# Kernel tuning notes

Measured on AMD Instinct MI355X. Metric: run time of the kernel, lower is better.

The kernel has to match this reference:

```python
import jax, jax.numpy as jnp
import numpy as np

B, N, C, H = 8192, 36, 128, 8
HD = C // H  # 16
FOCUS = 3
EPS = 1e-4


def setup_inputs() -> dict:
    key = jax.random.key(0)
    ks = jax.random.split(key, 10)
    x = jax.random.normal(ks[0], (B, N, C), dtype=jnp.float32)
    pos = jax.random.normal(ks[1], (B, N, C), dtype=jnp.float32)
    mask = jax.random.randint(ks[2], (B, N), 0, 2).astype(jnp.float32)
    coords = jax.random.randint(ks[3], (B * N, 4), 0, 8).astype(jnp.int64)
    voxel_inds = jax.random.permutation(ks[4], B * N).reshape(B, N).astype(jnp.int64)
    s = 0.02
    qk_w = jax.random.normal(ks[5], (C, 2 * C), dtype=jnp.float32) * s
    qk_b = jnp.zeros((2 * C,), dtype=jnp.float32)
    v_w = jax.random.normal(ks[6], (C, C), dtype=jnp.float32) * s
    v_b = jnp.zeros((C,), dtype=jnp.float32)
    proj_w = jax.random.normal(ks[7], (C, C), dtype=jnp.float32) * s
    proj_b = jnp.zeros((C,), dtype=jnp.float32)
    return {"x": x, "pos": pos, "mask": mask, "qk_w": qk_w, "qk_b": qk_b,
            "v_w": v_w, "v_b": v_b, "proj_w": proj_w, "proj_b": proj_b,
            "coords": coords, "voxel_inds": voxel_inds}


def reference(x, pos, mask, qk_w, qk_b, v_w, v_b, proj_w, proj_b, coords, voxel_inds):
    b, n, c = x.shape
    qk = (x + pos) @ qk_w + qk_b                      # (B,N,2C)
    q, k = qk[..., :c], qk[..., c:]
    v = x @ v_w + v_b                                 # (B,N,C)
    k = k * mask[..., None]
    # split heads -> (B,H,N,HD)
    q = q.reshape(b, n, H, HD).transpose(0, 2, 1, 3)
    k = k.reshape(b, n, H, HD).transpose(0, 2, 1, 3)
    v = v.reshape(b, n, H, HD).transpose(0, 2, 1, 3)
    # focusing power
    q = q ** FOCUS
    k = k ** FOCUS
    # q normalized per-token over channels; k normalized per-channel over tokens
    # (original rearranges k to (bh, c, n) before norm(dim=-1))
    q = q / (EPS + jnp.linalg.norm(q, axis=-1, keepdims=True))
    k = k / (EPS + jnp.linalg.norm(k, axis=2, keepdims=True))
    # linear attention: kv = k^T v (HD x HD), then q @ kv
    kv = jnp.einsum('bhnc,bhnd->bhcd', k, v)          # (B,H,HD,HD)
    out = jnp.einsum('bhnc,bhcd->bhnd', q, kv)        # (B,H,N,HD)
    out = out.transpose(0, 2, 1, 3).reshape(b, n, c)  # (B,N,C)
    num = jnp.sum(mask, axis=-1, keepdims=True)       # (B,1)
    out = out / (num[..., None] + EPS)
    # inverse-permutation gather: perm[voxel_inds.flat] = arange
    flat = voxel_inds.reshape(-1)
    M = coords.shape[0]
    perm = jnp.zeros((M,), dtype=flat.dtype).at[flat].set(
        jnp.arange(M, dtype=flat.dtype))
    out = out.reshape(-1, c)[perm]                    # (M,C)
    out = out @ proj_w + proj_b
    return out
```

## Files before the change

### kernel.cpp

```cpp
#include <hip/hip_runtime.h>

typedef __bf16 bf16x8 __attribute__((ext_vector_type(8)));
typedef float f32x4 __attribute__((ext_vector_type(4)));

#define Bdim 8192
#define Nn 36
#define Cc 128
#define EPSf 1e-4f

#define WS_QK_HI 0
#define WS_QK_LO 32768
#define WS_V_HI  65536
#define WS_P_HI  81920

#define OFF_XH   0
#define OFF_PH   12288
#define OFF_PL   24576
#define OFF_KT   0
#define OFF_VT   12288
#define OFF_QH   24576
#define OFF_KV   33792
#define OFF_O    0
#define OFF_MASK 39936
#define OFF_VOX  40128
#define OFF_INN  40272
#define LDS_BYTES 40448

__device__ inline uint bfh(float f) {
    __bf16 h = (__bf16)f;
    return (uint)(*(const ushort*)&h);
}
__device__ inline uint bfl(float f) {
    float hf = (float)((__bf16)f);
    __bf16 l = (__bf16)(f - hf);
    return (uint)(*(const ushort*)&l);
}
__device__ inline uint pk2h(float a, float b) { return bfh(a) | (bfh(b) << 16); }
__device__ inline uint pk2l(float a, float b) { return bfl(a) | (bfl(b) << 16); }

union U8 { bf16x8 v; uint u[4]; };

__global__ __launch_bounds__(256)
void prep_frags(const float* __restrict__ qk_w, const float* __restrict__ v_w,
                const float* __restrict__ proj_w, ushort* __restrict__ ws)
{
    int e = blockIdx.x * 256 + threadIdx.x;
    const float* W; int N; int idx; int hi_off; int lo_off;
    if (e < 32768)      { W = qk_w;   N = 256; hi_off = WS_QK_HI; lo_off = WS_QK_LO; idx = e; }
    else if (e < 49152) { W = v_w;    N = 128; hi_off = WS_V_HI;  lo_off = -1;       idx = e - 32768; }
    else                { W = proj_w; N = 128; hi_off = WS_P_HI;  lo_off = -1;       idx = e - 49152; }
    int j    = idx & 7;
    int lane = (idx >> 3) & 63;
    int ks   = (idx >> 9) & 3;
    int ct   = idx >> 11;
    int col  = ct * 16 + (lane & 15);
    int k    = ks * 32 + (lane >> 4) * 8 + j;
    float v  = W[k * N + col];
    ws[hi_off + idx] = (ushort)bfh(v);
    if (lo_off >= 0) ws[lo_off + idx] = (ushort)bfl(v);
}

__global__ __launch_bounds__(512, 6)
void fla_mfma(const float* __restrict__ x, const float* __restrict__ pos,
              const float* __restrict__ mask, const float* __restrict__ qk_b,
              const float* __restrict__ v_b, const float* __restrict__ proj_b,
              const int* __restrict__ vox, const ushort* __restrict__ ws,
              float* __restrict__ out)
{
    __shared__ __align__(16) char lds[LDS_BYTES];
    const int t = threadIdx.x;
    const int b = blockIdx.x;
    const int lane = t & 63;
    const int wv = t >> 6;

    const int  rsel = lane & 15;
    const int  grp  = lane >> 4;
    const uint kgrp = (uint)grp * 8u;
    const uint sw   = ((uint)rsel) << 4;

    const float* xg = x + (size_t)b * (Nn * Cc);
    const float* pg = pos + (size_t)b * (Nn * Cc);
    #pragma unroll
    for (int it = 0; it < 3; ++it) {
        int idx = t + it * 512;
        int n = idx >> 5;
        int c4 = (idx & 31) << 2;
        float4 xv = make_float4(0.f, 0.f, 0.f, 0.f);
        float4 pv = make_float4(0.f, 0.f, 0.f, 0.f);
        if (n < Nn) {
            xv = *(const float4*)(xg + n * Cc + c4);
            pv = *(const float4*)(pg + n * Cc + c4);
        }
        float s0 = xv.x + pv.x, s1 = xv.y + pv.y, s2 = xv.z + pv.z, s3 = xv.w + pv.w;
        uint ba = (uint)n * 256u + (((uint)(c4 * 2)) ^ (((uint)n & 15u) << 4));
        *(uint2*)(lds + OFF_XH + ba) = make_uint2(pk2h(xv.x, xv.y), pk2h(xv.z, xv.w));
        *(uint2*)(lds + OFF_PH + ba) = make_uint2(pk2h(s0, s1), pk2h(s2, s3));
        *(uint2*)(lds + OFF_PL + ba) = make_uint2(pk2l(s0, s1), pk2l(s2, s3));
    }
    if (t < 48) ((float*)(lds + OFF_MASK))[t] = (t < Nn) ? mask[(size_t)b * Nn + t] : 0.f;
    if (t >= 64 && t < 64 + Nn) ((int*)(lds + OFF_VOX))[t - 64] = vox[(size_t)b * Nn + (t - 64)];
    if (t == 128) {
        float s = 0.f;
        for (int n = 0; n < Nn; ++n) s += mask[(size_t)b * Nn + n];
        *(float*)(lds + OFF_INN) = 1.f / (s + EPSf);
    }
    __syncthreads();

    f32x4 accV[3];
    f32x4 accQ[3][2];
    #pragma unroll
    for (int rt = 0; rt < 3; ++rt) {
        accV[rt] = (f32x4){0.f, 0.f, 0.f, 0.f};
        accQ[rt][0] = (f32x4){0.f, 0.f, 0.f, 0.f};
        accQ[rt][1] = (f32x4){0.f, 0.f, 0.f, 0.f};
    }
    #pragma unroll
    for (int ks = 0; ks < 4; ++ks) {
        uint ka = (((uint)(ks * 32) + kgrp) * 2u) ^ sw;
        bf16x8 xh[3];
        #pragma unroll
        for (int rt = 0; rt < 3; ++rt)
            xh[rt] = *(const bf16x8*)(lds + OFF_XH + (uint)(rt * 16 + rsel) * 256u + ka);
        int f = ((wv * 4 + ks) * 64 + lane) * 8;
        bf16x8 bvh = *(const bf16x8*)(ws + WS_V_HI + f);
        #pragma unroll
        for (int rt = 0; rt < 3; ++rt)
            accV[rt] = __builtin_amdgcn_mfma_f32_16x16x32_bf16(xh[rt], bvh, accV[rt], 0, 0, 0);
    }
    #pragma unroll
    for (int ks = 0; ks < 4; ++ks) {
        uint ka = (((uint)(ks * 32) + kgrp) * 2u) ^ sw;
        bf16x8 ph[3], pl[3];
        #pragma unroll
        for (int rt = 0; rt < 3; ++rt) {
            uint ba = (uint)(rt * 16 + rsel) * 256u + ka;
            ph[rt] = *(const bf16x8*)(lds + OFF_PH + ba);
            pl[rt] = *(const bf16x8*)(lds + OFF_PL + ba);
        }
        #pragma unroll
        for (int ci = 0; ci < 2; ++ci) {
            int f = (((wv * 2 + ci) * 4 + ks) * 64 + lane) * 8;
            bf16x8 bh = *(const bf16x8*)(ws + WS_QK_HI + f);
            bf16x8 bl = *(const bf16x8*)(ws + WS_QK_LO + f);
            #pragma unroll
            for (int rt = 0; rt < 3; ++rt) {
                accQ[rt][ci] = __builtin_amdgcn_mfma_f32_16x16x32_bf16(ph[rt], bh, accQ[rt][ci], 0, 0, 0);
                accQ[rt][ci] = __builtin_amdgcn_mfma_f32_16x16x32_bf16(ph[rt], bl, accQ[rt][ci], 0, 0, 0);
                accQ[rt][ci] = __builtin_amdgcn_mfma_f32_16x16x32_bf16(pl[rt], bh, accQ[rt][ci], 0, 0, 0);
            }
        }
    }
    __syncthreads();

    const float* sM = (const float*)(lds + OFF_MASK);
    {
        int colv = wv * 16 + rsel;
        float vb = v_b[colv];
        #pragma unroll
        for (int rt = 0; rt < 3; ++rt) {
            float a0 = accV[rt][0] + vb, a1 = accV[rt][1] + vb;
            float a2 = accV[rt][2] + vb, a3 = accV[rt][3] + vb;
            uint addr = OFF_VT + (uint)(colv * 48 + rt * 16 + grp * 4) * 2u;
            *(uint2*)(lds + addr) = make_uint2(pk2h(a0, a1), pk2h(a2, a3));
        }
    }
    if (wv < 4) {
        #pragma unroll
        for (int ci = 0; ci < 2; ++ci) {
            int colq = (wv * 2 + ci) * 16 + rsel;
            float qb = qk_b[colq];
            uint cb2 = (uint)(colq * 2);
            #pragma unroll
            for (int rt = 0; rt < 3; ++rt) {
                #pragma unroll
                for (int r = 0; r < 4; ++r) {
                    int row = rt * 16 + grp * 4 + r;
                    if (row < Nn) {
                        float q1 = accQ[rt][ci][r] + qb;
                        float q3 = q1 * q1 * q1;
                        uint ba = (uint)row * 256u + (cb2 ^ (((uint)row & 15u) << 4));
                        *(ushort*)(lds + OFF_QH + ba) = (ushort)bfh(q3);
                    }
                }
            }
        }
    } else {
        #pragma unroll
        for (int ci = 0; ci < 2; ++ci) {
            int colk = ((wv - 4) * 2 + ci) * 16 + rsel;
            float kb = qk_b[Cc + colk];
            #pragma unroll
            for (int rt = 0; rt < 3; ++rt) {
                float k3v[4];
                #pragma unroll
                for (int r = 0; r < 4; ++r) {
                    int row = rt * 16 + grp * 4 + r;
                    float k1 = (accQ[rt][ci][r] + kb) * sM[row];
                    k3v[r] = k1 * k1 * k1;
                }
                uint addr = OFF_KT + (uint)(colk * 48 + rt * 16 + grp * 4) * 2u;
                *(uint2*)(lds + addr) = make_uint2(pk2h(k3v[0], k3v[1]), pk2h(k3v[2], k3v[3]));
            }
        }
    }
    __syncthreads();

    {
        int col16 = wv * 16 + rsel;
        uint a0 = OFF_KT + (uint)(col16 * 48 + grp * 8) * 2u;
        uint b0 = OFF_VT + (uint)(col16 * 48 + grp * 8) * 2u;
        bf16x8 kA0 = *(const bf16x8*)(lds + a0);
        bf16x8 vB0 = *(const bf16x8*)(lds + b0);
        U8 kA1, vB1;
        kA1.u[0] = kA1.u[1] = kA1.u[2] = kA1.u[3] = 0u;
        vB1.u[0] = vB1.u[1] = vB1.u[2] = vB1.u[3] = 0u;
        if (grp < 2) {
            kA1.v = *(const bf16x8*)(lds + a0 + 64);
            vB1.v = *(const bf16x8*)(lds + b0 + 64);
        }
        float s = 0.f;
        #pragma unroll
        for (int j = 0; j < 8; ++j) { float q = (float)kA0[j]; s += q * q; }
        #pragma unroll
        for (int j = 0; j < 8; ++j) { float q = (float)kA1.v[j]; s += q * q; }
        s += __shfl_xor(s, 16);
        s += __shfl_xor(s, 32);
        float invkn = 1.f / (EPSf + sqrtf(s));

        f32x4 kvacc = (f32x4){0.f, 0.f, 0.f, 0.f};
        kvacc = __builtin_amdgcn_mfma_f32_16x16x32_bf16(kA0, vB0, kvacc, 0, 0, 0);
        kvacc = __builtin_amdgcn_mfma_f32_16x16x32_bf16(kA1.v, vB1.v, kvacc, 0, 0, 0);

        float f0 = __shfl(invkn, grp * 4 + 0);
        float f1 = __shfl(invkn, grp * 4 + 1);
        float f2 = __shfl(invkn, grp * 4 + 2);
        float f3 = __shfl(invkn, grp * 4 + 3);
        uint addr = OFF_KV + (uint)(wv * 384 + rsel * 24 + grp * 4) * 2u;
        *(uint2*)(lds + addr) =
            make_uint2(pk2h(kvacc[0] * f0, kvacc[1] * f1), pk2h(kvacc[2] * f2, kvacc[3] * f3));
    }
    __syncthreads();

    {
        int d = rsel;
        float inn = *(const float*)(lds + OFF_INN);
        U8 bkv;
        bkv.u[0] = bkv.u[1] = bkv.u[2] = bkv.u[3] = 0u;
        if (grp < 2)
            bkv.v = *(const bf16x8*)(lds + OFF_KV + (uint)(wv * 384 + d * 24 + grp * 8) * 2u);
        f32x4 oacc[3];
        float invn[3];
        #pragma unroll
        for (int rt = 0; rt < 3; ++rt) {
            int row = rt * 16 + rsel;
            U8 aq;
            aq.u[0] = aq.u[1] = aq.u[2] = aq.u[3] = 0u;
            if (grp < 2 && row < Nn) {
                uint ba = (uint)row * 256u +
                          (((uint)((wv * 16 + grp * 8) * 2)) ^ (((uint)row & 15u) << 4));
                aq.v = *(const bf16x8*)(lds + OFF_QH + ba);
            }
            float s = 0.f;
            #pragma unroll
            for (int j = 0; j < 8; ++j) { float q = (float)aq.v[j]; s += q * q; }
            s += __shfl_xor(s, 16);
            invn[rt] = 1.f / (EPSf + sqrtf(s));
            f32x4 o = (f32x4){0.f, 0.f, 0.f, 0.f};
            o = __builtin_amdgcn_mfma_f32_16x16x32_bf16(aq.v, bkv.v, o, 0, 0, 0);
            oacc[rt] = o;
        }
        #pragma unroll
        for (int rt = 0; rt < 3; ++rt) {
            #pragma unroll
            for (int r = 0; r < 4; ++r) {
                int rr = grp * 4 + r;
                int row = rt * 16 + rr;
                float fac = __shfl(invn[rt], rr) * inn;
                float val = oacc[rt][r] * fac;
                uint ba = (uint)row * 256u +
                          (((uint)((wv * 16 + d) * 2)) ^ (((uint)row & 15u) << 4));
                *(ushort*)(lds + OFF_O + ba) = (ushort)bfh(val);
            }
        }
    }
    __syncthreads();

    f32x4 accP[3];
    #pragma unroll
    for (int rt = 0; rt < 3; ++rt) accP[rt] = (f32x4){0.f, 0.f, 0.f, 0.f};
    #pragma unroll
    for (int ks = 0; ks < 4; ++ks) {
        uint ka = (((uint)(ks * 32) + kgrp) * 2u) ^ sw;
        bf16x8 oa[3];
        #pragma unroll
        for (int rt = 0; rt < 3; ++rt)
            oa[rt] = *(const bf16x8*)(lds + OFF_O + (uint)(rt * 16 + rsel) * 256u + ka);
        int f = ((wv * 4 + ks) * 64 + lane) * 8;
        bf16x8 bp = *(const bf16x8*)(ws + WS_P_HI + f);
        #pragma unroll
        for (int rt = 0; rt < 3; ++rt)
            accP[rt] = __builtin_amdgcn_mfma_f32_16x16x32_bf16(oa[rt], bp, accP[rt], 0, 0, 0);
    }
    {
        const int* sVx = (const int*)(lds + OFF_VOX);
        int col = wv * 16 + rsel;
        float pb = proj_b[col];
        #pragma unroll
        for (int rt = 0; rt < 3; ++rt) {
            #pragma unroll
            for (int r = 0; r < 4; ++r) {
                int row = rt * 16 + grp * 4 + r;
                if (row < Nn)
                    out[(size_t)sVx[row] * Cc + col] = accP[rt][r] + pb;
            }
        }
    }
}

extern "C" void kernel_launch(void* const* d_in, const int* in_sizes, int n_in,
                              void* d_out, int out_size, void* d_ws, size_t ws_size,
                              hipStream_t stream) {
    (void)in_sizes; (void)n_in; (void)out_size; (void)ws_size;
    const float* x      = (const float*)d_in[0];
    const float* pos    = (const float*)d_in[1];
    const float* mask   = (const float*)d_in[2];
    const float* qk_w   = (const float*)d_in[3];
    const float* qk_b   = (const float*)d_in[4];
    const float* v_w    = (const float*)d_in[5];
    const float* v_b    = (const float*)d_in[6];
    const float* proj_w = (const float*)d_in[7];
    const float* proj_b = (const float*)d_in[8];
    const int*   vox    = (const int*)d_in[10];
    ushort* ws = (ushort*)d_ws;
    float* outp = (float*)d_out;

    hipLaunchKernelGGL(prep_frags, dim3(256), dim3(256), 0, stream, qk_w, v_w, proj_w, ws);
    hipLaunchKernelGGL(fla_mfma, dim3(Bdim), dim3(512), 0, stream,
                       x, pos, mask, qk_b, v_b, proj_b, vox, ws, outp);
}
```

Before: 218.9 us.

## Process two batches per block with staggered double-buffered LDS phases

Each block now handles two batch items, each with its own LDS buffer, and interleaves their phases so one item's global loads and MFMA work overlap the other's epilogue stages. This halves the grid and shares barriers across both items, reducing per-item sync cost. The KV scratch stride shrinks to fit two buffers, padding rows are zeroed once up front, and launch bounds drop to 4 waves per SIMD, trading occupancy and register pressure for in-block overlap.

```diff
diff --git a/kernel.cpp b/kernel.cpp
--- a/kernel.cpp
+++ b/kernel.cpp
@@ -21,10 +21,10 @@
 #define OFF_QH   24576
 #define OFF_KV   33792
 #define OFF_O    0
-#define OFF_MASK 39936
-#define OFF_VOX  40128
-#define OFF_INN  40272
-#define LDS_BYTES 40448
+#define OFF_MASK 38912
+#define OFF_VOX  39104
+#define OFF_INN  39248
+#define AST      39296
 
 __device__ inline uint bfh(float f) {
     __bf16 h = (__bf16)f;
@@ -60,16 +60,15 @@
     if (lo_off >= 0) ws[lo_off + idx] = (ushort)bfl(v);
 }
 
-__global__ __launch_bounds__(512, 6)
+__global__ __launch_bounds__(512, 4)
 void fla_mfma(const float* __restrict__ x, const float* __restrict__ pos,
               const float* __restrict__ mask, const float* __restrict__ qk_b,
               const float* __restrict__ v_b, const float* __restrict__ proj_b,
               const int* __restrict__ vox, const ushort* __restrict__ ws,
               float* __restrict__ out)
 {
-    __shared__ __align__(16) char lds[LDS_BYTES];
+    __shared__ __align__(16) char lds[2][AST];
     const int t = threadIdx.x;
-    const int b = blockIdx.x;
     const int lane = t & 63;
     const int wv = t >> 6;
 
@@ -78,145 +77,152 @@
     const uint kgrp = (uint)grp * 8u;
     const uint sw   = ((uint)rsel) << 4;
 
-    const float* xg = x + (size_t)b * (Nn * Cc);
-    const float* pg = pos + (size_t)b * (Nn * Cc);
-    #pragma unroll
-    for (int it = 0; it < 3; ++it) {
-        int idx = t + it * 512;
-        int n = idx >> 5;
-        int c4 = (idx & 31) << 2;
-        float4 xv = make_float4(0.f, 0.f, 0.f, 0.f);
-        float4 pv = make_float4(0.f, 0.f, 0.f, 0.f);
-        if (n < Nn) {
-            xv = *(const float4*)(xg + n * Cc + c4);
-            pv = *(const float4*)(pg + n * Cc + c4);
-        }
-        float s0 = xv.x + pv.x, s1 = xv.y + pv.y, s2 = xv.z + pv.z, s3 = xv.w + pv.w;
-        uint ba = (uint)n * 256u + (((uint)(c4 * 2)) ^ (((uint)n & 15u) << 4));
-        *(uint2*)(lds + OFF_XH + ba) = make_uint2(pk2h(xv.x, xv.y), pk2h(xv.z, xv.w));
-        *(uint2*)(lds + OFF_PH + ba) = make_uint2(pk2h(s0, s1), pk2h(s2, s3));
-        *(uint2*)(lds + OFF_PL + ba) = make_uint2(pk2l(s0, s1), pk2l(s2, s3));
-    }
-    if (t < 48) ((float*)(lds + OFF_MASK))[t] = (t < Nn) ? mask[(size_t)b * Nn + t] : 0.f;
-    if (t >= 64 && t < 64 + Nn) ((int*)(lds + OFF_VOX))[t - 64] = vox[(size_t)b * Nn + (t - 64)];
-    if (t == 128) {
-        float s = 0.f;
-        for (int n = 0; n < Nn; ++n) s += mask[(size_t)b * Nn + n];
-        *(float*)(lds + OFF_INN) = 1.f / (s + EPSf);
-    }
-    __syncthreads();
-
-    f32x4 accV[3];
-    f32x4 accQ[3][2];
-    #pragma unroll
-    for (int rt = 0; rt < 3; ++rt) {
-        accV[rt] = (f32x4){0.f, 0.f, 0.f, 0.f};
-        accQ[rt][0] = (f32x4){0.f, 0.f, 0.f, 0.f};
-        accQ[rt][1] = (f32x4){0.f, 0.f, 0.f, 0.f};
-    }
-    #pragma unroll
-    for (int ks = 0; ks < 4; ++ks) {
-        uint ka = (((uint)(ks * 32) + kgrp) * 2u) ^ sw;
-        bf16x8 xh[3];
-        #pragma unroll
-        for (int rt = 0; rt < 3; ++rt)
-            xh[rt] = *(const bf16x8*)(lds + OFF_XH + (uint)(rt * 16 + rsel) * 256u + ka);
-        int f = ((wv * 4 + ks) * 64 + lane) * 8;
-        bf16x8 bvh = *(const bf16x8*)(ws + WS_V_HI + f);
-        #pragma unroll
-        for (int rt = 0; rt < 3; ++rt)
-            accV[rt] = __builtin_amdgcn_mfma_f32_16x16x32_bf16(xh[rt], bvh, accV[rt], 0, 0, 0);
-    }
-    #pragma unroll
-    for (int ks = 0; ks < 4; ++ks) {
-        uint ka = (((uint)(ks * 32) + kgrp) * 2u) ^ sw;
-        bf16x8 ph[3], pl[3];
+    const int b0 = blockIdx.x * 2;
+    const int b1 = b0 + 1;
+
+    auto PA = [&](int ar, int bb) {
+        char* L = lds[ar];
+        const float* xg = x + (size_t)bb * (Nn * Cc);
+        const float* pg = pos + (size_t)bb * (Nn * Cc);
+        #pragma unroll
+        for (int it = 0; it < 3; ++it) {
+            int idx = t + it * 512;
+            if (idx < Nn * 32) {
+                int n = idx >> 5;
+                int c4 = (idx & 31) << 2;
+                float4 xv = *(const float4*)(xg + n * Cc + c4);
+                float4 pv = *(const float4*)(pg + n * Cc + c4);
+                float s0 = xv.x + pv.x, s1 = xv.y + pv.y;
+                float s2 = xv.z + pv.z, s3 = xv.w + pv.w;
+                uint ba = (uint)n * 256u + (((uint)(c4 * 2)) ^ (((uint)n & 15u) << 4));
+                *(uint2*)(L + OFF_XH + ba) = make_uint2(pk2h(xv.x, xv.y), pk2h(xv.z, xv.w));
+                *(uint2*)(L + OFF_PH + ba) = make_uint2(pk2h(s0, s1), pk2h(s2, s3));
+                *(uint2*)(L + OFF_PL + ba) = make_uint2(pk2l(s0, s1), pk2l(s2, s3));
+            }
+        }
+        if (t < 48) ((float*)(L + OFF_MASK))[t] = (t < Nn) ? mask[(size_t)bb * Nn + t] : 0.f;
+        if (t >= 64 && t < 64 + Nn) ((int*)(L + OFF_VOX))[t - 64] = vox[(size_t)bb * Nn + (t - 64)];
+        if (t == 128) {
+            float s = 0.f;
+            for (int n = 0; n < Nn; ++n) s += mask[(size_t)bb * Nn + n];
+            *(float*)(L + OFF_INN) = 1.f / (s + EPSf);
+        }
+    };
+
+    auto PB = [&](int ar, f32x4 (&accV)[3], f32x4 (&accQ)[3][2]) {
+        char* L = lds[ar];
         #pragma unroll
         for (int rt = 0; rt < 3; ++rt) {
-            uint ba = (uint)(rt * 16 + rsel) * 256u + ka;
-            ph[rt] = *(const bf16x8*)(lds + OFF_PH + ba);
-            pl[rt] = *(const bf16x8*)(lds + OFF_PL + ba);
-        }
-        #pragma unroll
-        for (int ci = 0; ci < 2; ++ci) {
-            int f = (((wv * 2 + ci) * 4 + ks) * 64 + lane) * 8;
-            bf16x8 bh = *(const bf16x8*)(ws + WS_QK_HI + f);
-            bf16x8 bl = *(const bf16x8*)(ws + WS_QK_LO + f);
+            accV[rt] = (f32x4){0.f, 0.f, 0.f, 0.f};
+            accQ[rt][0] = (f32x4){0.f, 0.f, 0.f, 0.f};
+            accQ[rt][1] = (f32x4){0.f, 0.f, 0.f, 0.f};
+        }
+        #pragma unroll
+        for (int ks = 0; ks < 4; ++ks) {
+            uint ka = (((uint)(ks * 32) + kgrp) * 2u) ^ sw;
+            bf16x8 xh[3];
+            #pragma unroll
+            for (int rt = 0; rt < 3; ++rt)
+                xh[rt] = *(const bf16x8*)(L + OFF_XH + (uint)(rt * 16 + rsel) * 256u + ka);
+            int f = ((wv * 4 + ks) * 64 + lane) * 8;
+            bf16x8 bvh = *(const bf16x8*)(ws + WS_V_HI + f);
+            #pragma unroll
+            for (int rt = 0; rt < 3; ++rt)
+                accV[rt] = __builtin_amdgcn_mfma_f32_16x16x32_bf16(xh[rt], bvh, accV[rt], 0, 0, 0);
+        }
+        #pragma unroll
+        for (int ks = 0; ks < 4; ++ks) {
+            uint ka = (((uint)(ks * 32) + kgrp) * 2u) ^ sw;
+            bf16x8 ph[3], pl[3];
             #pragma unroll
             for (int rt = 0; rt < 3; ++rt) {
-                accQ[rt][ci] = __builtin_amdgcn_mfma_f32_16x16x32_bf16(ph[rt], bh, accQ[rt][ci], 0, 0, 0);
-                accQ[rt][ci] = __builtin_amdgcn_mfma_f32_16x16x32_bf16(ph[rt], bl, accQ[rt][ci], 0, 0, 0);
-                accQ[rt][ci] = __builtin_amdgcn_mfma_f32_16x16x32_bf16(pl[rt], bh, accQ[rt][ci], 0, 0, 0);
-            }
-        }
-    }
-    __syncthreads();
-
-    const float* sM = (const float*)(lds + OFF_MASK);
-    {
-        int colv = wv * 16 + rsel;
-        float vb = v_b[colv];
-        #pragma unroll
-        for (int rt = 0; rt < 3; ++rt) {
-            float a0 = accV[rt][0] + vb, a1 = accV[rt][1] + vb;
-            float a2 = accV[rt][2] + vb, a3 = accV[rt][3] + vb;
-            uint addr = OFF_VT + (uint)(colv * 48 + rt * 16 + grp * 4) * 2u;
-            *(uint2*)(lds + addr) = make_uint2(pk2h(a0, a1), pk2h(a2, a3));
-        }
-    }
-    if (wv < 4) {
-        #pragma unroll
-        for (int ci = 0; ci < 2; ++ci) {
-            int colq = (wv * 2 + ci) * 16 + rsel;
-            float qb = qk_b[colq];
-            uint cb2 = (uint)(colq * 2);
+                uint ba = (uint)(rt * 16 + rsel) * 256u + ka;
+                ph[rt] = *(const bf16x8*)(L + OFF_PH + ba);
+                pl[rt] = *(const bf16x8*)(L + OFF_PL + ba);
+            }
+            #pragma unroll
+            for (int ci = 0; ci < 2; ++ci) {
+                int f = (((wv * 2 + ci) * 4 + ks) * 64 + lane) * 8;
+                bf16x8 bh = *(const bf16x8*)(ws + WS_QK_HI + f);
+                bf16x8 bl = *(const bf16x8*)(ws + WS_QK_LO + f);
+                #pragma unroll
+                for (int rt = 0; rt < 3; ++rt) {
+                    accQ[rt][ci] = __builtin_amdgcn_mfma_f32_16x16x32_bf16(ph[rt], bh, accQ[rt][ci], 0, 0, 0);
+                    accQ[rt][ci] = __builtin_amdgcn_mfma_f32_16x16x32_bf16(ph[rt], bl, accQ[rt][ci], 0, 0, 0);
+                    accQ[rt][ci] = __builtin_amdgcn_mfma_f32_16x16x32_bf16(pl[rt], bh, accQ[rt][ci], 0, 0, 0);
+                }
+            }
+        }
+    };
+
+    auto PC = [&](int ar, f32x4 (&accV)[3], f32x4 (&accQ)[3][2]) {
+        char* L = lds[ar];
+        const float* sM = (const float*)(L + OFF_MASK);
+        {
+            int colv = wv * 16 + rsel;
+            float vb = v_b[colv];
             #pragma unroll
             for (int rt = 0; rt < 3; ++rt) {
+                float a0 = accV[rt][0] + vb, a1 = accV[rt][1] + vb;
+                float a2 = accV[rt][2] + vb, a3 = accV[rt][3] + vb;
+                uint addr = OFF_VT + (uint)(colv * 48 + rt * 16 + grp * 4) * 2u;
+                *(uint2*)(L + addr) = make_uint2(pk2h(a0, a1), pk2h(a2, a3));
+            }
+        }
+        if (wv < 4) {
+            #pragma unroll
+            for (int ci = 0; ci < 2; ++ci) {
+                int colq = (wv * 2 + ci) * 16 + rsel;
+                float qb = qk_b[colq];
+                uint cb2 = (uint)(colq * 2);
                 #pragma unroll
-                for (int r = 0; r < 4; ++r) {
-                    int row = rt * 16 + grp * 4 + r;
-                    if (row < Nn) {
-                        float q1 = accQ[rt][ci][r] + qb;
-                        float q3 = q1 * q1 * q1;
-                        uint ba = (uint)row * 256u + (cb2 ^ (((uint)row & 15u) << 4));
-                        *(ushort*)(lds + OFF_QH + ba) = (ushort)bfh(q3);
+                for (int rt = 0; rt < 3; ++rt) {
+                    #pragma unroll
+                    for (int r = 0; r < 4; ++r) {
+                        int row = rt * 16 + grp * 4 + r;
+                        if (row < Nn) {
+                            float q1 = accQ[rt][ci][r] + qb;
+                            float q3 = q1 * q1 * q1;
+                            uint ba = (uint)row * 256u + (cb2 ^ (((uint)row & 15u) << 4));
+                            *(ushort*)(L + OFF_QH + ba) = (ushort)bfh(q3);
+                        }
                     }
                 }
             }
-        }
-    } else {
-        #pragma unroll
-        for (int ci = 0; ci < 2; ++ci) {
-            int colk = ((wv - 4) * 2 + ci) * 16 + rsel;
-            float kb = qk_b[Cc + colk];
-            #pragma unroll
-            for (int rt = 0; rt < 3; ++rt) {
-                float k3v[4];
+        } else {
+            #pragma unroll
+            for (int ci = 0; ci < 2; ++ci) {
+                int colk = ((wv - 4) * 2 + ci) * 16 + rsel;
+                float kb = qk_b[Cc + colk];
                 #pragma unroll
-                for (int r = 0; r < 4; ++r) {
-                    int row = rt * 16 + grp * 4 + r;
-                    float k1 = (accQ[rt][ci][r] + kb) * sM[row];
-                    k3v[r] = k1 * k1 * k1;
+                for (int rt = 0; rt < 3; ++rt) {
+                    float k3v[4];
+                    #pragma unroll
+                    for (int r = 0; r < 4; ++r) {
+                        int row = rt * 16 + grp * 4 + r;
+                        float k1 = (accQ[rt][ci][r] + kb) * sM[row];
+                        k3v[r] = k1 * k1 * k1;
+                    }
+                    uint addr = OFF_KT + (uint)(colk * 48 + rt * 16 + grp * 4) * 2u;
+                    *(uint2*)(L + addr) = make_uint2(pk2h(k3v[0], k3v[1]), pk2h(k3v[2], k3v[3]));
                 }
-                uint addr = OFF_KT + (uint)(colk * 48 + rt * 16 + grp * 4) * 2u;
-                *(uint2*)(lds + addr) = make_uint2(pk2h(k3v[0], k3v[1]), pk2h(k3v[2], k3v[3]));
-            }
-        }
-    }
-    __syncthreads();
-
-    {
+            }
+        }
+    };
+
+    auto PD = [&](int ar) {
+        char* L = lds[ar];
         int col16 = wv * 16 + rsel;
         uint a0 = OFF_KT + (uint)(col16 * 48 + grp * 8) * 2u;
-        uint b0 = OFF_VT + (uint)(col16 * 48 + grp * 8) * 2u;
-        bf16x8 kA0 = *(const bf16x8*)(lds + a0);
-        bf16x8 vB0 = *(const bf16x8*)(lds + b0);
+        uint b0_ = OFF_VT + (uint)(col16 * 48 + grp * 8) * 2u;
+        bf16x8 kA0 = *(const bf16x8*)(L + a0);
+        bf16x8 vB0 = *(const bf16x8*)(L + b0_);
         U8 kA1, vB1;
         kA1.u[0] = kA1.u[1] = kA1.u[2] = kA1.u[3] = 0u;
         vB1.u[0] = vB1.u[1] = vB1.u[2] = vB1.u[3] = 0u;
         if (grp < 2) {
-            kA1.v = *(const bf16x8*)(lds + a0 + 64);
-            vB1.v = *(const bf16x8*)(lds + b0 + 64);
+            kA1.v = *(const bf16x8*)(L + a0 + 64);
+            vB1.v = *(const bf16x8*)(L + b0_ + 64);
         }
         float s = 0.f;
         #pragma unroll
@@ -235,19 +241,19 @@
         float f1 = __shfl(invkn, grp * 4 + 1);
         float f2 = __shfl(invkn, grp * 4 + 2);
         float f3 = __shfl(invkn, grp * 4 + 3);
-        uint addr = OFF_KV + (uint)(wv * 384 + rsel * 24 + grp * 4) * 2u;
-        *(uint2*)(lds + addr) =
+        uint addr = OFF_KV + (uint)(wv * 320 + rsel * 20 + grp * 4) * 2u;
+        *(uint2*)(L + addr) =
             make_uint2(pk2h(kvacc[0] * f0, kvacc[1] * f1), pk2h(kvacc[2] * f2, kvacc[3] * f3));
-    }
-    __syncthreads();
-
-    {
+    };
+
+    auto PE = [&](int ar) {
+        char* L = lds[ar];
         int d = rsel;
-        float inn = *(const float*)(lds + OFF_INN);
+        float inn = *(const float*)(L + OFF_INN);
         U8 bkv;
         bkv.u[0] = bkv.u[1] = bkv.u[2] = bkv.u[3] = 0u;
         if (grp < 2)
-            bkv.v = *(const bf16x8*)(lds + OFF_KV + (uint)(wv * 384 + d * 24 + grp * 8) * 2u);
+            bkv.v = *(const bf16x8*)(L + OFF_KV + (uint)(wv * 320 + d * 20 + grp * 8) * 2u);
         f32x4 oacc[3];
         float invn[3];
         #pragma unroll
@@ -258,7 +264,7 @@
             if (grp < 2 && row < Nn) {
                 uint ba = (uint)row * 256u +
                           (((uint)((wv * 16 + grp * 8) * 2)) ^ (((uint)row & 15u) << 4));
-                aq.v = *(const bf16x8*)(lds + OFF_QH + ba);
+                aq.v = *(const bf16x8*)(L + OFF_QH + ba);
             }
             float s = 0.f;
             #pragma unroll
@@ -279,30 +285,30 @@
                 float val = oacc[rt][r] * fac;
                 uint ba = (uint)row * 256u +
                           (((uint)((wv * 16 + d) * 2)) ^ (((uint)row & 15u) << 4));
-                *(ushort*)(lds + OFF_O + ba) = (ushort)bfh(val);
-            }
-        }
-    }
-    __syncthreads();
-
-    f32x4 accP[3];
-    #pragma unroll
-    for (int rt = 0; rt < 3; ++rt) accP[rt] = (f32x4){0.f, 0.f, 0.f, 0.f};
-    #pragma unroll
-    for (int ks = 0; ks < 4; ++ks) {
-        uint ka = (((uint)(ks * 32) + kgrp) * 2u) ^ sw;
-        bf16x8 oa[3];
-        #pragma unroll
-        for (int rt = 0; rt < 3; ++rt)
-            oa[rt] = *(const bf16x8*)(lds + OFF_O + (uint)(rt * 16 + rsel) * 256u + ka);
-        int f = ((wv * 4 + ks) * 64 + lane) * 8;
-        bf16x8 bp = *(const bf16x8*)(ws + WS_P_HI + f);
-        #pragma unroll
-        for (int rt = 0; rt < 3; ++rt)
-            accP[rt] = __builtin_amdgcn_mfma_f32_16x16x32_bf16(oa[rt], bp, accP[rt], 0, 0, 0);
-    }
-    {
-        const int* sVx = (const int*)(lds + OFF_VOX);
+                *(ushort*)(L + OFF_O + ba) = (ushort)bfh(val);
+            }
+        }
+    };
+
+    auto PG = [&](int ar) {
+        char* L = lds[ar];
+        f32x4 accP[3];
+        #pragma unroll
+        for (int rt = 0; rt < 3; ++rt) accP[rt] = (f32x4){0.f, 0.f, 0.f, 0.f};
+        #pragma unroll
+        for (int ks = 0; ks < 4; ++ks) {
+            uint ka = (((uint)(ks * 32) + kgrp) * 2u) ^ sw;
+            bf16x8 oa[3];
+            #pragma unroll
+            for (int rt = 0; rt < 3; ++rt)
+                oa[rt] = *(const bf16x8*)(L + OFF_O + (uint)(rt * 16 + rsel) * 256u + ka);
+            int f = ((wv * 4 + ks) * 64 + lane) * 8;
+            bf16x8 bp = *(const bf16x8*)(ws + WS_P_HI + f);
+            #pragma unroll
+            for (int rt = 0; rt < 3; ++rt)
+                accP[rt] = __builtin_amdgcn_mfma_f32_16x16x32_bf16(oa[rt], bp, accP[rt], 0, 0, 0);
+        }
+        const int* sVx = (const int*)(L + OFF_VOX);
         int col = wv * 16 + rsel;
         float pb = proj_b[col];
         #pragma unroll
@@ -314,7 +320,37 @@
                     out[(size_t)sVx[row] * Cc + col] = accP[rt][r] + pb;
             }
         }
+    };
+
+    f32x4 accV0[3], accV1[3];
+    f32x4 accQ0[3][2], accQ1[3][2];
+
+    for (int i = t; i < 1152; i += 512) {
+        int ar = (i >= 576) ? 1 : 0;
+        int r3 = i - ar * 576;
+        char* rp = lds[ar] + (r3 < 192 ? OFF_XH : (r3 < 384 ? OFF_PH : OFF_PL));
+        int off = (r3 % 192) * 16 - (r3 < 192 ? 0 : (r3 < 384 ? 192 * 16 : 384 * 16)) + (r3 % 192) * 0;
+        off = ((r3 % 192) * 16);
+        *(uint4*)(rp + 9216 + off) = make_uint4(0u, 0u, 0u, 0u);
     }
+    PA(0, b0);
+    __syncthreads();
+    PB(0, accV0, accQ0);
+    PA(1, b1);
+    __syncthreads();
+    PC(0, accV0, accQ0);
+    PB(1, accV1, accQ1);
+    __syncthreads();
+    PD(0);
+    PC(1, accV1, accQ1);
+    __syncthreads();
+    PE(0);
+    PD(1);
+    __syncthreads();
+    PG(0);
+    PE(1);
+    __syncthreads();
+    PG(1);
 }
 
 extern "C" void kernel_launch(void* const* d_in, const int* in_sizes, int n_in,
@@ -335,6 +371,6 @@
     float* outp = (float*)d_out;
 
     hipLaunchKernelGGL(prep_frags, dim3(256), dim3(256), 0, stream, qk_w, v_w, proj_w, ws);
-    hipLaunchKernelGGL(fla_mfma, dim3(Bdim), dim3(512), 0, stream,
+    hipLaunchKernelGGL(fla_mfma, dim3(Bdim / 2), dim3(512), 0, stream,
                        x, pos, mask, qk_b, v_b, proj_b, vox, ws, outp);
 }
```

Measured after the change: 203.6 us. 7.0% less time.

## Halve block to 4 waves, double per-wave tiles, fuse kv and output stages

Applied to the files above, without the earlier changes.

Shrinks the fused attention block from 8 to 4 waves, so each wave computes twice as many column tiles in the QK, V and projection GEMMs and handles two heads in the attention step. The kv matrix is passed between lanes with shuffles instead of through shared memory, which removes one barrier and one LDS round trip. Padding rows are zeroed explicitly and the K/V transposed stride goes from 48 to 52 to reduce bank conflicts. The cost is more registers per thread and fewer waves per block to hide latency, though the launch bounds allow more blocks per CU.

```diff
diff --git a/kernel.cpp b/kernel.cpp
--- a/kernel.cpp
+++ b/kernel.cpp
@@ -17,10 +17,8 @@
 #define OFF_PH   12288
 #define OFF_PL   24576
 #define OFF_KT   0
-#define OFF_VT   12288
-#define OFF_QH   24576
-#define OFF_KV   33792
-#define OFF_O    0
+#define OFF_VT   13312
+#define OFF_QO   27648
 #define OFF_MASK 39936
 #define OFF_VOX  40128
 #define OFF_INN  40272
@@ -60,7 +58,7 @@
     if (lo_off >= 0) ws[lo_off + idx] = (ushort)bfl(v);
 }
 
-__global__ __launch_bounds__(512, 6)
+__global__ __launch_bounds__(256, 4)
 void fla_mfma(const float* __restrict__ x, const float* __restrict__ pos,
               const float* __restrict__ mask, const float* __restrict__ qk_b,
               const float* __restrict__ v_b, const float* __restrict__ proj_b,
@@ -72,7 +70,6 @@
     const int b = blockIdx.x;
     const int lane = t & 63;
     const int wv = t >> 6;
-
     const int  rsel = lane & 15;
     const int  grp  = lane >> 4;
     const uint kgrp = (uint)grp * 8u;
@@ -81,21 +78,31 @@
     const float* xg = x + (size_t)b * (Nn * Cc);
     const float* pg = pos + (size_t)b * (Nn * Cc);
     #pragma unroll
-    for (int it = 0; it < 3; ++it) {
-        int idx = t + it * 512;
-        int n = idx >> 5;
-        int c4 = (idx & 31) << 2;
-        float4 xv = make_float4(0.f, 0.f, 0.f, 0.f);
-        float4 pv = make_float4(0.f, 0.f, 0.f, 0.f);
-        if (n < Nn) {
-            xv = *(const float4*)(xg + n * Cc + c4);
-            pv = *(const float4*)(pg + n * Cc + c4);
-        }
-        float s0 = xv.x + pv.x, s1 = xv.y + pv.y, s2 = xv.z + pv.z, s3 = xv.w + pv.w;
-        uint ba = (uint)n * 256u + (((uint)(c4 * 2)) ^ (((uint)n & 15u) << 4));
-        *(uint2*)(lds + OFF_XH + ba) = make_uint2(pk2h(xv.x, xv.y), pk2h(xv.z, xv.w));
-        *(uint2*)(lds + OFF_PH + ba) = make_uint2(pk2h(s0, s1), pk2h(s2, s3));
-        *(uint2*)(lds + OFF_PL + ba) = make_uint2(pk2l(s0, s1), pk2l(s2, s3));
+    for (int i0 = 0; i0 < 3; ++i0) {
+        int i = t + i0 * 256;
+        if (i < 576) {
+            int reg = i / 192;
+            int j = i - reg * 192;
+            int row = 36 + (j >> 4);
+            int c16 = j & 15;
+            *(uint4*)(lds + reg * 12288 + row * 256 + c16 * 16) = make_uint4(0u, 0u, 0u, 0u);
+        }
+    }
+    #pragma unroll
+    for (int it = 0; it < 5; ++it) {
+        int idx = t + it * 256;
+        if (idx < Nn * 32) {
+            int n = idx >> 5;
+            int c4 = (idx & 31) << 2;
+            float4 xv = *(const float4*)(xg + n * Cc + c4);
+            float4 pv = *(const float4*)(pg + n * Cc + c4);
+            float s0 = xv.x + pv.x, s1 = xv.y + pv.y;
+            float s2 = xv.z + pv.z, s3 = xv.w + pv.w;
+            uint ba = (uint)n * 256u + (((uint)(c4 * 2)) ^ (((uint)n & 15u) << 4));
+            *(uint2*)(lds + OFF_XH + ba) = make_uint2(pk2h(xv.x, xv.y), pk2h(xv.z, xv.w));
+            *(uint2*)(lds + OFF_PH + ba) = make_uint2(pk2h(s0, s1), pk2h(s2, s3));
+            *(uint2*)(lds + OFF_PL + ba) = make_uint2(pk2l(s0, s1), pk2l(s2, s3));
+        }
     }
     if (t < 48) ((float*)(lds + OFF_MASK))[t] = (t < Nn) ? mask[(size_t)b * Nn + t] : 0.f;
     if (t >= 64 && t < 64 + Nn) ((int*)(lds + OFF_VOX))[t - 64] = vox[(size_t)b * Nn + (t - 64)];
@@ -106,26 +113,14 @@
     }
     __syncthreads();
 
-    f32x4 accV[3];
-    f32x4 accQ[3][2];
+    f32x4 accQ[3][4];
+    f32x4 accV[3][2];
     #pragma unroll
     for (int rt = 0; rt < 3; ++rt) {
-        accV[rt] = (f32x4){0.f, 0.f, 0.f, 0.f};
-        accQ[rt][0] = (f32x4){0.f, 0.f, 0.f, 0.f};
-        accQ[rt][1] = (f32x4){0.f, 0.f, 0.f, 0.f};
-    }
-    #pragma unroll
-    for (int ks = 0; ks < 4; ++ks) {
-        uint ka = (((uint)(ks * 32) + kgrp) * 2u) ^ sw;
-        bf16x8 xh[3];
-        #pragma unroll
-        for (int rt = 0; rt < 3; ++rt)
-            xh[rt] = *(const bf16x8*)(lds + OFF_XH + (uint)(rt * 16 + rsel) * 256u + ka);
-        int f = ((wv * 4 + ks) * 64 + lane) * 8;
-        bf16x8 bvh = *(const bf16x8*)(ws + WS_V_HI + f);
-        #pragma unroll
-        for (int rt = 0; rt < 3; ++rt)
-            accV[rt] = __builtin_amdgcn_mfma_f32_16x16x32_bf16(xh[rt], bvh, accV[rt], 0, 0, 0);
+        #pragma unroll
+        for (int ci = 0; ci < 4; ++ci) accQ[rt][ci] = (f32x4){0.f, 0.f, 0.f, 0.f};
+        accV[rt][0] = (f32x4){0.f, 0.f, 0.f, 0.f};
+        accV[rt][1] = (f32x4){0.f, 0.f, 0.f, 0.f};
     }
     #pragma unroll
     for (int ks = 0; ks < 4; ++ks) {
@@ -138,8 +133,8 @@
             pl[rt] = *(const bf16x8*)(lds + OFF_PL + ba);
         }
         #pragma unroll
-        for (int ci = 0; ci < 2; ++ci) {
-            int f = (((wv * 2 + ci) * 4 + ks) * 64 + lane) * 8;
+        for (int ci = 0; ci < 4; ++ci) {
+            int f = (((wv * 4 + ci) * 4 + ks) * 64 + lane) * 8;
             bf16x8 bh = *(const bf16x8*)(ws + WS_QK_HI + f);
             bf16x8 bl = *(const bf16x8*)(ws + WS_QK_LO + f);
             #pragma unroll
@@ -150,24 +145,43 @@
             }
         }
     }
+    #pragma unroll
+    for (int ks = 0; ks < 4; ++ks) {
+        uint ka = (((uint)(ks * 32) + kgrp) * 2u) ^ sw;
+        bf16x8 xh[3];
+        #pragma unroll
+        for (int rt = 0; rt < 3; ++rt)
+            xh[rt] = *(const bf16x8*)(lds + OFF_XH + (uint)(rt * 16 + rsel) * 256u + ka);
+        #pragma unroll
+        for (int ci = 0; ci < 2; ++ci) {
+            int f = (((wv * 2 + ci) * 4 + ks) * 64 + lane) * 8;
+            bf16x8 bvh = *(const bf16x8*)(ws + WS_V_HI + f);
+            #pragma unroll
+            for (int rt = 0; rt < 3; ++rt)
+                accV[rt][ci] = __builtin_amdgcn_mfma_f32_16x16x32_bf16(xh[rt], bvh, accV[rt][ci], 0, 0, 0);
+        }
+    }
     __syncthreads();
 
     const float* sM = (const float*)(lds + OFF_MASK);
     {
-        int colv = wv * 16 + rsel;
-        float vb = v_b[colv];
-        #pragma unroll
-        for (int rt = 0; rt < 3; ++rt) {
-            float a0 = accV[rt][0] + vb, a1 = accV[rt][1] + vb;
-            float a2 = accV[rt][2] + vb, a3 = accV[rt][3] + vb;
-            uint addr = OFF_VT + (uint)(colv * 48 + rt * 16 + grp * 4) * 2u;
-            *(uint2*)(lds + addr) = make_uint2(pk2h(a0, a1), pk2h(a2, a3));
-        }
-    }
-    if (wv < 4) {
         #pragma unroll
         for (int ci = 0; ci < 2; ++ci) {
-            int colq = (wv * 2 + ci) * 16 + rsel;
+            int colv = (wv * 2 + ci) * 16 + rsel;
+            float vb = v_b[colv];
+            #pragma unroll
+            for (int rt = 0; rt < 3; ++rt) {
+                float a0 = accV[rt][ci][0] + vb, a1 = accV[rt][ci][1] + vb;
+                float a2 = accV[rt][ci][2] + vb, a3 = accV[rt][ci][3] + vb;
+                uint addr = OFF_VT + (uint)(colv * 52 + rt * 16 + grp * 4) * 2u;
+                *(uint2*)(lds + addr) = make_uint2(pk2h(a0, a1), pk2h(a2, a3));
+            }
+        }
+    }
+    if (wv < 2) {
+        #pragma unroll
+        for (int ci = 0; ci < 4; ++ci) {
+            int colq = (wv * 4 + ci) * 16 + rsel;
             float qb = qk_b[colq];
             uint cb2 = (uint)(colq * 2);
             #pragma unroll
@@ -179,15 +193,15 @@
                         float q1 = accQ[rt][ci][r] + qb;
                         float q3 = q1 * q1 * q1;
                         uint ba = (uint)row * 256u + (cb2 ^ (((uint)row & 15u) << 4));
-                        *(ushort*)(lds + OFF_QH + ba) = (ushort)bfh(q3);
+                        *(ushort*)(lds + OFF_QO + ba) = (ushort)bfh(q3);
                     }
                 }
             }
         }
     } else {
         #pragma unroll
-        for (int ci = 0; ci < 2; ++ci) {
-            int colk = ((wv - 4) * 2 + ci) * 16 + rsel;
+        for (int ci = 0; ci < 4; ++ci) {
+            int colk = ((wv - 2) * 4 + ci) * 16 + rsel;
             float kb = qk_b[Cc + colk];
             #pragma unroll
             for (int rt = 0; rt < 3; ++rt) {
@@ -198,7 +212,7 @@
                     float k1 = (accQ[rt][ci][r] + kb) * sM[row];
                     k3v[r] = k1 * k1 * k1;
                 }
-                uint addr = OFF_KT + (uint)(colk * 48 + rt * 16 + grp * 4) * 2u;
+                uint addr = OFF_KT + (uint)(colk * 52 + rt * 16 + grp * 4) * 2u;
                 *(uint2*)(lds + addr) = make_uint2(pk2h(k3v[0], k3v[1]), pk2h(k3v[2], k3v[3]));
             }
         }
@@ -206,112 +220,142 @@
     __syncthreads();
 
     {
-        int col16 = wv * 16 + rsel;
-        uint a0 = OFF_KT + (uint)(col16 * 48 + grp * 8) * 2u;
-        uint b0 = OFF_VT + (uint)(col16 * 48 + grp * 8) * 2u;
-        bf16x8 kA0 = *(const bf16x8*)(lds + a0);
-        bf16x8 vB0 = *(const bf16x8*)(lds + b0);
-        U8 kA1, vB1;
-        kA1.u[0] = kA1.u[1] = kA1.u[2] = kA1.u[3] = 0u;
-        vB1.u[0] = vB1.u[1] = vB1.u[2] = vB1.u[3] = 0u;
-        if (grp < 2) {
-            kA1.v = *(const bf16x8*)(lds + a0 + 64);
-            vB1.v = *(const bf16x8*)(lds + b0 + 64);
-        }
-        float s = 0.f;
-        #pragma unroll
-        for (int j = 0; j < 8; ++j) { float q = (float)kA0[j]; s += q * q; }
-        #pragma unroll
-        for (int j = 0; j < 8; ++j) { float q = (float)kA1.v[j]; s += q * q; }
-        s += __shfl_xor(s, 16);
-        s += __shfl_xor(s, 32);
-        float invkn = 1.f / (EPSf + sqrtf(s));
-
-        f32x4 kvacc = (f32x4){0.f, 0.f, 0.f, 0.f};
-        kvacc = __builtin_amdgcn_mfma_f32_16x16x32_bf16(kA0, vB0, kvacc, 0, 0, 0);
-        kvacc = __builtin_amdgcn_mfma_f32_16x16x32_bf16(kA1.v, vB1.v, kvacc, 0, 0, 0);
-
-        float f0 = __shfl(invkn, grp * 4 + 0);
-        float f1 = __shfl(invkn, grp * 4 + 1);
-        float f2 = __shfl(invkn, grp * 4 + 2);
-        float f3 = __shfl(invkn, grp * 4 + 3);
-        uint addr = OFF_KV + (uint)(wv * 384 + rsel * 24 + grp * 4) * 2u;
-        *(uint2*)(lds + addr) =
-            make_uint2(pk2h(kvacc[0] * f0, kvacc[1] * f1), pk2h(kvacc[2] * f2, kvacc[3] * f3));
+        uint bkvU[2][4];
+        #pragma unroll
+        for (int hh = 0; hh < 2; ++hh) {
+            int h = wv * 2 + hh;
+            int col16 = h * 16 + rsel;
+            uint a0 = OFF_KT + (uint)(col16 * 52 + grp * 8) * 2u;
+            uint b0 = OFF_VT + (uint)(col16 * 52 + grp * 8) * 2u;
+            bf16x8 kA0 = *(const bf16x8*)(lds + a0);
+            bf16x8 vB0 = *(const bf16x8*)(lds + b0);
+            U8 kA1, vB1;
+            kA1.u[0] = kA1.u[1] = kA1.u[2] = kA1.u[3] = 0u;
+            vB1.u[0] = vB1.u[1] = vB1.u[2] = vB1.u[3] = 0u;
+            if (grp < 2) {
+                kA1.v = *(const bf16x8*)(lds + a0 + 64);
+                vB1.v = *(const bf16x8*)(lds + b0 + 64);
+            }
+            float s = 0.f;
+            #pragma unroll
+            for (int j = 0; j < 8; ++j) { float q = (float)kA0[j]; s += q * q; }
+            #pragma unroll
+            for (int j = 0; j < 8; ++j) { float q = (float)kA1.v[j]; s += q * q; }
+            s += __shfl_xor(s, 16);
+            s += __shfl_xor(s, 32);
+            float invkn = 1.f / (EPSf + sqrtf(s));
+
+            f32x4 kvacc = (f32x4){0.f, 0.f, 0.f, 0.f};
+            kvacc = __builtin_amdgcn_mfma_f32_16x16x32_bf16(kA0, vB0, kvacc, 0, 0, 0);
+            kvacc = __builtin_amdgcn_mfma_f32_16x16x32_bf16(kA1.v, vB1.v, kvacc, 0, 0, 0);
+            #pragma unroll
+            for (int r = 0; r < 4; ++r)
+                kvacc[r] *= __shfl(invkn, grp * 4 + r);
+
+            float bv[8];
+            #pragma unroll
+            for (int j = 0; j < 8; ++j)
+                bv[j] = __shfl(kvacc[j & 3], rsel + 16 * (2 * grp + (j >> 2)));
+            if (grp >= 2) {
+                #pragma unroll
+                for (int j = 0; j < 8; ++j) bv[j] = 0.f;
+            }
+            bkvU[hh][0] = pk2h(bv[0], bv[1]);
+            bkvU[hh][1] = pk2h(bv[2], bv[3]);
+            bkvU[hh][2] = pk2h(bv[4], bv[5]);
+            bkvU[hh][3] = pk2h(bv[6], bv[7]);
+        }
+
+        float inn = *(const float*)(lds + OFF_INN);
+        U8 aq[2][3];
+        #pragma unroll
+        for (int hh = 0; hh < 2; ++hh) {
+            uint cb = (uint)((wv * 2 + hh) * 32 + grp * 16);
+            #pragma unroll
+            for (int rt = 0; rt < 3; ++rt) {
+                int row = rt * 16 + rsel;
+                aq[hh][rt].u[0] = aq[hh][rt].u[1] = aq[hh][rt].u[2] = aq[hh][rt].u[3] = 0u;
+                if (grp < 2 && row < Nn)
+                    aq[hh][rt].v = *(const bf16x8*)(lds + OFF_QO + (uint)row * 256u + (cb ^ sw));
+            }
+        }
+        f32x4 oacc[2][3];
+        float invn[2][3];
+        #pragma unroll
+        for (int hh = 0; hh < 2; ++hh) {
+            U8 bkv;
+            bkv.u[0] = bkvU[hh][0]; bkv.u[1] = bkvU[hh][1];
+            bkv.u[2] = bkvU[hh][2]; bkv.u[3] = bkvU[hh][3];
+            #pragma unroll
+            for (int rt = 0; rt < 3; ++rt) {
+                float s = 0.f;
+                #pragma unroll
+                for (int j = 0; j < 8; ++j) { float q = (float)aq[hh][rt].v[j]; s += q * q; }
+                s += __shfl_xor(s, 16);
+                invn[hh][rt] = 1.f / (EPSf + sqrtf(s));
+                f32x4 o = (f32x4){0.f, 0.f, 0.f, 0.f};
+                o = __builtin_amdgcn_mfma_f32_16x16x32_bf16(aq[hh][rt].v, bkv.v, o, 0, 0, 0);
+                oacc[hh][rt] = o;
+            }
+        }
+        #pragma unroll
+        for (int hh = 0; hh < 2; ++hh) {
+            int h = wv * 2 + hh;
+            uint cb2 = (uint)((h * 16 + rsel) * 2);
+            #pragma unroll
+            for (int rt = 0; rt < 3; ++rt) {
+                #pragma unroll
+                for (int r = 0; r < 4; ++r) {
+                    int rr = grp * 4 + r;
+                    int row = rt * 16 + rr;
+                    if (row < Nn) {
+                        float fac = __shfl(invn[hh][rt], rr) * inn;
+                        float val = oacc[hh][rt][r] * fac;
+                        uint ba = (uint)row * 256u + (cb2 ^ (((uint)row & 15u) << 4));
+                        *(ushort*)(lds + OFF_QO + ba) = (ushort)bfh(val);
+                    }
+                }
+            }
+        }
     }
     __syncthreads();
 
-    {
-        int d = rsel;
-        float inn = *(const float*)(lds + OFF_INN);
-        U8 bkv;
-        bkv.u[0] = bkv.u[1] = bkv.u[2] = bkv.u[3] = 0u;
-        if (grp < 2)
-            bkv.v = *(const bf16x8*)(lds + OFF_KV + (uint)(wv * 384 + d * 24 + grp * 8) * 2u);
-        f32x4 oacc[3];
-        float invn[3];
-        #pragma unroll
-        for (int rt = 0; rt < 3; ++rt) {
-            int row = rt * 16 + rsel;
-            U8 aq;
-            aq.u[0] = aq.u[1] = aq.u[2] = aq.u[3] = 0u;
-            if (grp < 2 && row < Nn) {
-                uint ba = (uint)row * 256u +
-                          (((uint)((wv * 16 + grp * 8) * 2)) ^ (((uint)row & 15u) << 4));
-                aq.v = *(const bf16x8*)(lds + OFF_QH + ba);
-            }
-            float s = 0.f;
-            #pragma unroll
-            for (int j = 0; j < 8; ++j) { float q = (float)aq.v[j]; s += q * q; }
-            s += __shfl_xor(s, 16);
-            invn[rt] = 1.f / (EPSf + sqrtf(s));
-            f32x4 o = (f32x4){0.f, 0.f, 0.f, 0.f};
-            o = __builtin_amdgcn_mfma_f32_16x16x32_bf16(aq.v, bkv.v, o, 0, 0, 0);
-            oacc[rt] = o;
-        }
-        #pragma unroll
-        for (int rt = 0; rt < 3; ++rt) {
-            #pragma unroll
-            for (int r = 0; r < 4; ++r) {
-                int rr = grp * 4 + r;
-                int row = rt * 16 + rr;
-                float fac = __shfl(invn[rt], rr) * inn;
-                float val = oacc[rt][r] * fac;
-                uint ba = (uint)row * 256u +
-                          (((uint)((wv * 16 + d) * 2)) ^ (((uint)row & 15u) << 4));
-                *(ushort*)(lds + OFF_O + ba) = (ushort)bfh(val);
-            }
-        }
-    }
-    __syncthreads();
-
-    f32x4 accP[3];
-    #pragma unroll
-    for (int rt = 0; rt < 3; ++rt) accP[rt] = (f32x4){0.f, 0.f, 0.f, 0.f};
+    f32x4 accP[3][2];
+    #pragma unroll
+    for (int rt = 0; rt < 3; ++rt) {
+        accP[rt][0] = (f32x4){0.f, 0.f, 0.f, 0.f};
+        accP[rt][1] = (f32x4){0.f, 0.f, 0.f, 0.f};
+    }
     #pragma unroll
     for (int ks = 0; ks < 4; ++ks) {
         uint ka = (((uint)(ks * 32) + kgrp) * 2u) ^ sw;
         bf16x8 oa[3];
         #pragma unroll
         for (int rt = 0; rt < 3; ++rt)
-            oa[rt] = *(const bf16x8*)(lds + OFF_O + (uint)(rt * 16 + rsel) * 256u + ka);
-        int f = ((wv * 4 + ks) * 64 + lane) * 8;
-        bf16x8 bp = *(const bf16x8*)(ws + WS_P_HI + f);
-        #pragma unroll
-        for (int rt = 0; rt < 3; ++rt)
-            accP[rt] = __builtin_amdgcn_mfma_f32_16x16x32_bf16(oa[rt], bp, accP[rt], 0, 0, 0);
+            oa[rt] = *(const bf16x8*)(lds + OFF_QO + (uint)(rt * 16 + rsel) * 256u + ka);
+        #pragma unroll
+        for (int ci = 0; ci < 2; ++ci) {
+            int f = (((wv * 2 + ci) * 4 + ks) * 64 + lane) * 8;
+            bf16x8 bp = *(const bf16x8*)(ws + WS_P_HI + f);
+            #pragma unroll
+            for (int rt = 0; rt < 3; ++rt)
+                accP[rt][ci] = __builtin_amdgcn_mfma_f32_16x16x32_bf16(oa[rt], bp, accP[rt][ci], 0, 0, 0);
+        }
     }
     {
         const int* sVx = (const int*)(lds + OFF_VOX);
-        int col = wv * 16 + rsel;
-        float pb = proj_b[col];
-        #pragma unroll
-        for (int rt = 0; rt < 3; ++rt) {
-            #pragma unroll
-            for (int r = 0; r < 4; ++r) {
-                int row = rt * 16 + grp * 4 + r;
-                if (row < Nn)
-                    out[(size_t)sVx[row] * Cc + col] = accP[rt][r] + pb;
+        #pragma unroll
+        for (int ci = 0; ci < 2; ++ci) {
+            int col = (wv * 2 + ci) * 16 + rsel;
+            float pb = proj_b[col];
+            #pragma unroll
+            for (int rt = 0; rt < 3; ++rt) {
+                #pragma unroll
+                for (int r = 0; r < 4; ++r) {
+                    int row = rt * 16 + grp * 4 + r;
+                    if (row < Nn)
+                        out[(size_t)sVx[row] * Cc + col] = accP[rt][ci][r] + pb;
+                }
             }
         }
     }
@@ -335,6 +379,6 @@
     float* outp = (float*)d_out;
 
     hipLaunchKernelGGL(prep_frags, dim3(256), dim3(256), 0, stream, qk_w, v_w, proj_w, ws);
-    hipLaunchKernelGGL(fla_mfma, dim3(Bdim), dim3(512), 0, stream,
+    hipLaunchKernelGGL(fla_mfma, dim3(Bdim), dim3(256), 0, stream,
                        x, pos, mask, qk_b, v_b, proj_b, vox, ws, outp);
 }
```

Result: faster. 212.3 us (-3.0%).
